# Kernel tuning notes

Hardware: AMD Instinct MI355X
Metric: run time of the kernel (lower is better)

## Reference

```python
import jax, jax.numpy as jnp
import numpy as np
import math

GROUPS = 32
HEADS = 8
EPS_GN = 1e-5


def group_norm(x, w, b):
    # x: [B, C, H, W]; GroupNorm32 computes in float32
    B, C, H, W = x.shape
    xg = x.astype(jnp.float32).reshape(B, GROUPS, C // GROUPS, H, W)
    mu = xg.mean(axis=(2, 3, 4), keepdims=True)
    var = xg.var(axis=(2, 3, 4), keepdims=True)
    xn = (xg - mu) * jax.lax.rsqrt(var + EPS_GN)
    xn = xn.reshape(B, C, H, W)
    return (xn * w[None, :, None, None] + b[None, :, None, None]).astype(x.dtype)


def fresnel_interference(H, W, wavelength):
    ys, xs = jnp.meshgrid(jnp.arange(H, dtype=jnp.float32),
                          jnp.arange(W, dtype=jnp.float32), indexing='ij')
    pos = jnp.stack([ys, xs], axis=-1).reshape(-1, 2)  # [N, 2]
    diff = pos[None, :, :] - pos[:, None, :]           # [N, N, 2]
    dist = jnp.sqrt((diff ** 2).sum(-1) + 1e-8)        # [N, N]
    phase = 2.0 * math.pi * dist / (jnp.abs(wavelength) * H + 1e-6)
    return jnp.cos(phase)


def fresnel_attn(h, qkv_w, out_w, out_b, wavelength):
    B, C, H, W = h.shape
    N = H * W
    dh = C // HEADS
    scale = dh ** -0.5
    xf = h.reshape(B, C, N).transpose(0, 2, 1)                 # [B, N, C]
    qkv = xf @ qkv_w                                            # [B, N, 3C]
    q, k, v = jnp.split(qkv, 3, axis=-1)
    def heads(t):
        return t.reshape(B, N, HEADS, dh).transpose(0, 2, 1, 3)  # [B, Hh, N, dh]
    q, k, v = heads(q), heads(k), heads(v)
    dots = jnp.einsum('bhnd,bhmd->bhnm', q, k) * scale
    interference = fresnel_interference(H, W, wavelength)       # [N, N]
    dots = dots + interference[None, None] * 0.1
    attn = jax.nn.softmax(dots, axis=-1)
    out = jnp.einsum('bhnm,bhmd->bhnd', attn, v)
    out = out.transpose(0, 2, 1, 3).reshape(B, N, C)
    out = out @ out_w + out_b
    return out.transpose(0, 2, 1).reshape(B, C, H, W)


def cross_attn(h, context, q_w, k_w, v_w, out_w, out_b):
    B, C, H, W = h.shape
    N = H * W
    inner = q_w.shape[1]
    dh = inner // HEADS
    scale = dh ** -0.5
    xf = h.reshape(B, C, N).transpose(0, 2, 1)                 # [B, N, C]
    q = xf @ q_w                                                # [B, N, inner]
    k = context @ k_w                                           # [B, L, inner]
    v = context @ v_w
    L = context.shape[1]
    q = q.reshape(B, N, HEADS, dh).transpose(0, 2, 1, 3)
    k = k.reshape(B, L, HEADS, dh).transpose(0, 2, 1, 3)
    v = v.reshape(B, L, HEADS, dh).transpose(0, 2, 1, 3)
    attn = jax.nn.softmax(jnp.einsum('bhnd,bhld->bhnl', q, k) * scale, axis=-1)
    out = jnp.einsum('bhnl,bhld->bhnd', attn, v)
    out = out.transpose(0, 2, 1, 3).reshape(B, N, inner)
    out = out @ out_w + out_b
    return out.transpose(0, 2, 1).reshape(B, C, H, W)


def setup_inputs() -> dict:
    key = jax.random.key(0)
    ks = jax.random.split(key, 10)
    B, C, H, W = 4, 512, 32, 32
    ctx_len, ctx_dim = 77, 768
    s = lambda d: 1.0 / math.sqrt(d)
    return {
        'x': jax.random.normal(ks[0], (B, C, H, W), jnp.float32),
        'context': jax.random.normal(ks[1], (B, ctx_len, ctx_dim), jnp.float32),
        'gn1_w': jnp.ones((C,), jnp.float32),
        'gn1_b': jnp.zeros((C,), jnp.float32),
        'gn2_w': jnp.ones((C,), jnp.float32),
        'gn2_b': jnp.zeros((C,), jnp.float32),
        'fa_qkv_w': jax.random.normal(ks[2], (C, 3 * C), jnp.float32) * s(C),
        'fa_out_w': jax.random.normal(ks[3], (C, C), jnp.float32) * s(C),
        'fa_out_b': jnp.zeros((C,), jnp.float32),
        'wavelength': jnp.asarray(0.1, jnp.float32),
        'ca_q_w': jax.random.normal(ks[4], (C, 512), jnp.float32) * s(C),
        'ca_k_w': jax.random.normal(ks[5], (ctx_dim, 512), jnp.float32) * s(ctx_dim),
        'ca_v_w': jax.random.normal(ks[6], (ctx_dim, 512), jnp.float32) * s(ctx_dim),
        'ca_out_w': jax.random.normal(ks[7], (512, C), jnp.float32) * s(512),
        'ca_out_b': jnp.zeros((C,), jnp.float32),
    }


def reference(x, context, gn1_w, gn1_b, gn2_w, gn2_b,
              fa_qkv_w, fa_out_w, fa_out_b, wavelength,
              ca_q_w, ca_k_w, ca_v_w, ca_out_w, ca_out_b):
    h = group_norm(x, gn1_w, gn1_b)
    h = fresnel_attn(h, fa_qkv_w, fa_out_w, fa_out_b, wavelength)
    x = x + h
    h = group_norm(x, gn2_w, gn2_b)
    h = cross_attn(h, context, ca_q_w, ca_k_w, ca_v_w, ca_out_w, ca_out_b)
    return x + h
```

## Files before the change

### kernel.cpp

```cpp
#include <hip/hip_runtime.h>
#include <hip/hip_bf16.h>
#include <math.h>

#define B_    4
#define N_    1024
#define L_    77

typedef float f4 __attribute__((ext_vector_type(4)));
typedef short bf8 __attribute__((ext_vector_type(8)));
typedef short s4v __attribute__((ext_vector_type(4)));

#if __has_builtin(__builtin_amdgcn_exp2f)
#define EXP2(x) __builtin_amdgcn_exp2f(x)
#else
#define EXP2(x) exp2f(x)
#endif

__device__ __forceinline__ float fs(short s) {
    unsigned u = ((unsigned)(unsigned short)s) << 16;
    return __builtin_bit_cast(float, u);
}
__device__ __forceinline__ short sf(float f) {
    unsigned u = __builtin_bit_cast(unsigned, f);
    unsigned r = (u + 0x7FFF + ((u >> 16) & 1)) >> 16;
    return (short)r;
}
__device__ __forceinline__ bf8 zero8() { bf8 v; for (int i = 0; i < 8; ++i) v[i] = 0; return v; }
__device__ __forceinline__ f4 zerof4() { f4 v; for (int i = 0; i < 4; ++i) v[i] = 0.f; return v; }

#define MFMA(a, b, c) __builtin_amdgcn_mfma_f32_16x16x32_bf16((a), (b), (c), 0, 0, 0)

__device__ __forceinline__ void wtile(const float* __restrict__ in, short* __restrict__ out,
                                      int K, int J, int tile, int tid, float (*t)[33])
{
    int jt = J >> 5;
    int j0 = (tile % jt) * 32, k0 = (tile / jt) * 32;
    int tx = tid & 31, ty = tid >> 5;
#pragma unroll
    for (int i = 0; i < 4; ++i)
        t[ty + i * 8][tx] = in[(size_t)(k0 + ty + i * 8) * J + j0 + tx];
    __syncthreads();
#pragma unroll
    for (int i = 0; i < 4; ++i)
        out[(size_t)(j0 + ty + i * 8) * K + k0 + tx] = sf(t[tx][ty + i * 8]);
}

__global__ __launch_bounds__(256)
void prep_mega(const float* __restrict__ wl, short* __restrict__ tab,
               const float* __restrict__ qkvw, short* __restrict__ qkvwT,
               const float* __restrict__ faow, short* __restrict__ faowT,
               const float* __restrict__ caqw, short* __restrict__ caqwT,
               const float* __restrict__ cakw, short* __restrict__ cakwT,
               const float* __restrict__ cavw, short* __restrict__ cavwT,
               const float* __restrict__ caow, short* __restrict__ caowT,
               const float* __restrict__ ctx, short* __restrict__ ctxb)
{
    __shared__ float tls[32][33];
    int bid = blockIdx.x, tid = threadIdx.x;
    if (bid < 16) {
        int idx = bid * 256 + tid;
        if (idx < 3969) {
            int i = idx / 63, j = idx - i * 63;
            float dy = (float)(i - 31), dx = (float)(j - 31);
            float dist = sqrtf(dy * dy + dx * dx + 1e-8f);
            float den = fabsf(wl[0]) * 32.0f + 1e-6f;
            tab[idx] = sf(0.1f * cosf(6.283185307179586f * dist / den) * 1.4426950408889634f);
        }
        return;
    }
    bid -= 16;
    if (bid < 768) { wtile(qkvw, qkvwT, 512, 1536, bid, tid, tls); return; }
    bid -= 768;
    if (bid < 256) { wtile(faow, faowT, 512, 512, bid, tid, tls); return; }
    bid -= 256;
    if (bid < 256) { wtile(caqw, caqwT, 512, 512, bid, tid, tls); return; }
    bid -= 256;
    if (bid < 384) { wtile(cakw, cakwT, 768, 512, bid, tid, tls); return; }
    bid -= 384;
    if (bid < 384) { wtile(cavw, cavwT, 768, 512, bid, tid, tls); return; }
    bid -= 384;
    if (bid < 256) { wtile(caow, caowT, 512, 512, bid, tid, tls); return; }
    bid -= 256;
    int base = bid * 1024 + tid * 4;
    float4 v = *(const float4*)(ctx + base);
    s4v o; o[0] = sf(v.x); o[1] = sf(v.y); o[2] = sf(v.z); o[3] = sf(v.w);
    *(s4v*)(ctxb + base) = o;
}

__global__ __launch_bounds__(256)
void gn_fused(const float* __restrict__ src, const float* __restrict__ w,
              const float* __restrict__ bs, short* __restrict__ dst)
{
    int g = blockIdx.x, b = blockIdx.y;
    const float* xb = src + ((size_t)b * 512 + g * 16) * 1024;
    float s = 0.f, ss = 0.f;
    for (int l = threadIdx.x; l < 4096; l += 256) {
        float4 v = *(const float4*)(xb + l * 4);
        s += v.x + v.y + v.z + v.w;
        ss += v.x * v.x + v.y * v.y + v.z * v.z + v.w * v.w;
    }
    for (int off = 32; off; off >>= 1) {
        s  += __shfl_down(s,  off);
        ss += __shfl_down(ss, off);
    }
    __shared__ float sred[8], ssred[8];
    int wid = threadIdx.x >> 6;
    if ((threadIdx.x & 63) == 0) { sred[wid] = s; ssred[wid] = ss; }
    __syncthreads();
    if (threadIdx.x == 0) {
        float S = 0.f, SS = 0.f;
        for (int i = 0; i < 4; ++i) { S += sred[i]; SS += ssred[i]; }
        float mu = S * (1.f / 16384.f);
        float var = SS * (1.f / 16384.f) - mu * mu;
        sred[4] = mu; ssred[4] = rsqrtf(var + 1e-5f);
    }
    __syncthreads();
    float mu = sred[4], rs = ssred[4];

    int c4 = threadIdx.x & 3, nb = threadIdx.x >> 2;
    int c = g * 16 + c4 * 4;
    float4 wv = *(const float4*)(w + c);
    float4 bv = *(const float4*)(bs + c);
    for (int rep = 0; rep < 16; ++rep) {
        int n = rep * 64 + nb;
        float v0 = xb[(size_t)(c4 * 4 + 0) * 1024 + n];
        float v1 = xb[(size_t)(c4 * 4 + 1) * 1024 + n];
        float v2 = xb[(size_t)(c4 * 4 + 2) * 1024 + n];
        float v3 = xb[(size_t)(c4 * 4 + 3) * 1024 + n];
        s4v hb;
        hb[0] = sf((v0 - mu) * rs * wv.x + bv.x);
        hb[1] = sf((v1 - mu) * rs * wv.y + bv.y);
        hb[2] = sf((v2 - mu) * rs * wv.z + bv.z);
        hb[3] = sf((v3 - mu) * rs * wv.w + bv.w);
        *(s4v*)(dst + ((size_t)b * 1024 + n) * 512 + c) = hb;
    }
}

template<int EPI>
__global__ __launch_bounds__(256)
void gemm_mfma(const short* __restrict__ A, const short* __restrict__ Wt,
               const float* __restrict__ bias, const float* __restrict__ res,
               void* __restrict__ outv, void* __restrict__ out2v,
               int M, int K, int J,
               long aStride, long wStride, long oStride, long o2Stride)
{
    int j0 = blockIdx.x * 128, m0 = blockIdx.y * 128, b = blockIdx.z;
    __shared__ short As[2][128][40];
    __shared__ short Ws[2][128][40];
    int tid = threadIdx.x, w = tid >> 6, lane = tid & 63;
    int lr = lane & 15, lg = lane >> 4;
    int wr = w >> 1, wc = w & 1;
    const short* Ab  = A  + (size_t)b * aStride;
    const short* Wtb = Wt + (size_t)b * wStride;
    int r0 = tid >> 2, c0 = (tid & 3) * 8;
    int r1 = 64 + r0;
    bool gA0 = (m0 + r0) < M, gA1 = (m0 + r1) < M;
    const short* ap0 = Ab + (size_t)(m0 + r0) * K + c0;
    const short* ap1 = Ab + (size_t)(m0 + r1) * K + c0;
    const short* wp0 = Wtb + (size_t)(j0 + r0) * K + c0;
    const short* wp1 = Wtb + (size_t)(j0 + r1) * K + c0;

    f4 acc[4][4];
#pragma unroll
    for (int i = 0; i < 4; ++i)
#pragma unroll
        for (int j = 0; j < 4; ++j) acc[i][j] = zerof4();

    *(bf8*)&As[0][r0][c0] = gA0 ? *(const bf8*)ap0 : zero8();
    *(bf8*)&As[0][r1][c0] = gA1 ? *(const bf8*)ap1 : zero8();
    *(bf8*)&Ws[0][r0][c0] = *(const bf8*)wp0;
    *(bf8*)&Ws[0][r1][c0] = *(const bf8*)wp1;
    __syncthreads();

    int nk = K >> 5;
    for (int t = 0; t < nk; ++t) {
        int cur = t & 1;
        bool more = (t + 1) < nk;
        bf8 na0, na1, nw0, nw1;
        if (more) {
            int ko = (t + 1) << 5;
            na0 = gA0 ? *(const bf8*)(ap0 + ko) : zero8();
            na1 = gA1 ? *(const bf8*)(ap1 + ko) : zero8();
            nw0 = *(const bf8*)(wp0 + ko);
            nw1 = *(const bf8*)(wp1 + ko);
        }
        bf8 af[4], bfr[4];
#pragma unroll
        for (int fi = 0; fi < 4; ++fi)
            af[fi] = *(const bf8*)&As[cur][wr * 64 + fi * 16 + lr][lg * 8];
#pragma unroll
        for (int fj = 0; fj < 4; ++fj)
            bfr[fj] = *(const bf8*)&Ws[cur][wc * 64 + fj * 16 + lr][lg * 8];
#pragma unroll
        for (int fi = 0; fi < 4; ++fi)
#pragma unroll
            for (int fj = 0; fj < 4; ++fj)
                acc[fi][fj] = MFMA(af[fi], bfr[fj], acc[fi][fj]);
        if (more) {
            int nb = cur ^ 1;
            *(bf8*)&As[nb][r0][c0] = na0;
            *(bf8*)&As[nb][r1][c0] = na1;
            *(bf8*)&Ws[nb][r0][c0] = nw0;
            *(bf8*)&Ws[nb][r1][c0] = nw1;
        }
        __syncthreads();
    }

    if (EPI == 0) {
        short* out = (short*)outv + (size_t)b * oStride;
#pragma unroll
        for (int fi = 0; fi < 4; ++fi)
#pragma unroll
            for (int reg = 0; reg < 4; ++reg) {
                int m = m0 + wr * 64 + fi * 16 + lg * 4 + reg;
                if (m < M) {
#pragma unroll
                    for (int fj = 0; fj < 4; ++fj)
                        out[(size_t)m * J + j0 + wc * 64 + fj * 16 + lr] = sf(acc[fi][fj][reg]);
                }
            }
    } else if (EPI == 1) {
        float* out = (float*)outv + (size_t)b * oStride;
        const float* rp = res + (size_t)b * oStride;
#pragma unroll
        for (int fi = 0; fi < 4; ++fi) {
            float4 bq = *(const float4*)(bias + m0 + wr * 64 + fi * 16 + lg * 4);
            float bvr[4] = {bq.x, bq.y, bq.z, bq.w};
#pragma unroll
            for (int reg = 0; reg < 4; ++reg) {
                int m = m0 + wr * 64 + fi * 16 + lg * 4 + reg;
                size_t ro = (size_t)m * J + j0 + wc * 64;
#pragma unroll
                for (int fj = 0; fj < 4; ++fj) {
                    size_t idx = ro + fj * 16 + lr;
                    out[idx] = acc[fi][fj][reg] + bvr[reg] + rp[idx];
                }
            }
        }
    } else if (EPI == 3) {
        if (j0 < 1024) {
            short* out = (short*)outv + (size_t)b * oStride;
#pragma unroll
            for (int fi = 0; fi < 4; ++fi)
#pragma unroll
                for (int reg = 0; reg < 4; ++reg) {
                    int m = m0 + wr * 64 + fi * 16 + lg * 4 + reg;
#pragma unroll
                    for (int fj = 0; fj < 4; ++fj)
                        out[(size_t)m * 1024 + j0 + wc * 64 + fj * 16 + lr] = sf(acc[fi][fj][reg]);
                }
        } else {
            short* Vg = (short*)out2v + (size_t)b * o2Stride;
#pragma unroll
            for (int fi = 0; fi < 4; ++fi) {
                int n = m0 + wr * 64 + fi * 16 + lg * 4;
#pragma unroll
                for (int fj = 0; fj < 4; ++fj) {
                    int dg = j0 - 1024 + wc * 64 + fj * 16 + lr;
                    s4v v;
#pragma unroll
                    for (int reg = 0; reg < 4; ++reg) v[reg] = sf(acc[fi][fj][reg]);
                    *(s4v*)(Vg + (size_t)dg * 1024 + n) = v;
                }
            }
        }
    } else {
        if (j0 < 512) {
            short* out = (short*)outv + (size_t)b * oStride;
#pragma unroll
            for (int fi = 0; fi < 4; ++fi)
#pragma unroll
                for (int reg = 0; reg < 4; ++reg) {
                    int m = m0 + wr * 64 + fi * 16 + lg * 4 + reg;
                    if (m < M) {
#pragma unroll
                        for (int fj = 0; fj < 4; ++fj)
                            out[(size_t)m * 512 + j0 + wc * 64 + fj * 16 + lr] = sf(acc[fi][fj][reg]);
                    }
                }
        } else {
            short* vt = (short*)out2v + (size_t)b * o2Stride;
#pragma unroll
            for (int fi = 0; fi < 4; ++fi) {
                int l0 = wr * 64 + fi * 16 + lg * 4;
                if (l0 < 80) {
#pragma unroll
                    for (int fj = 0; fj < 4; ++fj) {
                        int dg = j0 - 512 + wc * 64 + fj * 16 + lr;
                        s4v v;
#pragma unroll
                        for (int reg = 0; reg < 4; ++reg) v[reg] = sf(acc[fi][fj][reg]);
                        *(s4v*)(vt + (size_t)dg * 80 + l0) = v;
                    }
                }
            }
        }
    }
}

__global__ __launch_bounds__(256)
void fresnel_attn_v2(const short* __restrict__ qkb, const short* __restrict__ Vg,
                     const short* __restrict__ tab, short* __restrict__ ao)
{
    int qb = blockIdx.x, h = blockIdx.y, b = blockIdx.z;
    int n0 = qb * 64;
    __shared__ short Ks[2][64][64];
    __shared__ short Vt[2][64][64];
    __shared__ short Ps[4][16][72];
    __shared__ short tabs[4032];
    int tid = threadIdx.x, w = tid >> 6, lane = tid & 63;
    int lr = lane & 15, lg = lane >> 4;
    const short* qp = qkb + (size_t)b * 1048576;
    const short* vp = Vg + ((size_t)b * 512 + h * 64) * 1024;

    for (int l = tid; l < 504; l += 256)
        *(bf8*)&tabs[l * 8] = *(const bf8*)(tab + l * 8);

    int q = n0 + w * 16 + lr;
    bf8 qf0 = *(const bf8*)(qp + (size_t)q * 1024 + h * 64 + lg * 8);
    bf8 qf1 = *(const bf8*)(qp + (size_t)q * 1024 + h * 64 + 32 + lg * 8);

    int sr0 = tid >> 3, sc0 = tid & 7;
    int sr1 = 32 + sr0;
    int sw0 = ((sc0 ^ (sr0 & 7))) * 8;
    int sw1 = ((sc0 ^ (sr1 & 7))) * 8;

    *(bf8*)&Ks[0][sr0][sw0] = *(const bf8*)(qp + (size_t)sr0 * 1024 + 512 + h * 64 + sc0 * 8);
    *(bf8*)&Ks[0][sr1][sw1] = *(const bf8*)(qp + (size_t)sr1 * 1024 + 512 + h * 64 + sc0 * 8);
    *(bf8*)&Vt[0][sr0][sw0] = *(const bf8*)(vp + (size_t)sr0 * 1024 + sc0 * 8);
    *(bf8*)&Vt[0][sr1][sw1] = *(const bf8*)(vp + (size_t)sr1 * 1024 + sc0 * 8);
    __syncthreads();

    float mrun = -1e30f, lrun = 0.f;
    f4 o[4];
#pragma unroll
    for (int i = 0; i < 4; ++i) o[i] = zerof4();

    int ybase = (q >> 5) + 31;
    int xbase = (q & 31) + 31 - lg * 4;
    int rsw = lr & 7;
    int rc0 = (lg ^ rsw) * 8;
    int rc1 = ((4 + lg) ^ rsw) * 8;

    for (int t = 0; t < 16; ++t) {
        int cur = t & 1;
        int m0 = t << 6;
        bool more = t < 15;
        bf8 nk0, nk1, nv0, nv1;
        if (more) {
            int m1 = m0 + 64;
            nk0 = *(const bf8*)(qp + (size_t)(m1 + sr0) * 1024 + 512 + h * 64 + sc0 * 8);
            nk1 = *(const bf8*)(qp + (size_t)(m1 + sr1) * 1024 + 512 + h * 64 + sc0 * 8);
            nv0 = *(const bf8*)(vp + (size_t)sr0 * 1024 + m1 + sc0 * 8);
            nv1 = *(const bf8*)(vp + (size_t)sr1 * 1024 + m1 + sc0 * 8);
        }

        f4 sa[4];
#pragma unroll
        for (int fj = 0; fj < 4; ++fj) sa[fj] = zerof4();
#pragma unroll
        for (int fj = 0; fj < 4; ++fj)
            sa[fj] = MFMA(*(const bf8*)&Ks[cur][fj * 16 + lr][rc0], qf0, sa[fj]);
#pragma unroll
        for (int fj = 0; fj < 4; ++fj)
            sa[fj] = MFMA(*(const bf8*)&Ks[cur][fj * 16 + lr][rc1], qf1, sa[fj]);

        int yb = ybase - (m0 >> 5);
        float pv[4][4];
        float tmax = -1e30f;
#pragma unroll
        for (int fj = 0; fj < 4; ++fj) {
            int rowoff = (yb - (fj >> 1)) * 63 + xbase - (fj & 1) * 16;
#pragma unroll
            for (int reg = 0; reg < 4; ++reg) {
                float t2 = fmaf(sa[fj][reg], 0.18033688011112042f, fs(tabs[rowoff - reg]));
                pv[fj][reg] = t2;
                tmax = fmaxf(tmax, t2);
            }
        }
        tmax = fmaxf(tmax, __shfl_xor(tmax, 16));
        tmax = fmaxf(tmax, __shfl_xor(tmax, 32));
        float mnew = fmaxf(mrun, tmax);
        float rsc = EXP2(mrun - mnew);
        mrun = mnew;
        float psum = 0.f;
#pragma unroll
        for (int fj = 0; fj < 4; ++fj) {
            s4v pw;
#pragma unroll
            for (int reg = 0; reg < 4; ++reg) {
                float p = EXP2(pv[fj][reg] - mnew);
                psum += p;
                pw[reg] = sf(p);
            }
            *(s4v*)&Ps[w][lr][fj * 16 + lg * 4] = pw;
        }
        psum += __shfl_xor(psum, 16);
        psum += __shfl_xor(psum, 32);
        lrun = lrun * rsc + psum;
#pragma unroll
        for (int fd = 0; fd < 4; ++fd)
#pragma unroll
            for (int reg = 0; reg < 4; ++reg) o[fd][reg] *= rsc;

        bf8 pa0 = *(const bf8*)&Ps[w][lr][lg * 8];
        bf8 pa1 = *(const bf8*)&Ps[w][lr][32 + lg * 8];
#pragma unroll
        for (int fd = 0; fd < 4; ++fd) {
            o[fd] = MFMA(*(const bf8*)&Vt[cur][fd * 16 + lr][rc0], pa0, o[fd]);
            o[fd] = MFMA(*(const bf8*)&Vt[cur][fd * 16 + lr][rc1], pa1, o[fd]);
        }

        if (more) {
            int nb = cur ^ 1;
            *(bf8*)&Ks[nb][sr0][sw0] = nk0;
            *(bf8*)&Ks[nb][sr1][sw1] = nk1;
            *(bf8*)&Vt[nb][sr0][sw0] = nv0;
            *(bf8*)&Vt[nb][sr1][sw1] = nv1;
        }
        __syncthreads();
    }

    float inv = 1.f / lrun;
    size_t rb = ((size_t)b * N_ + q) * 512 + h * 64;
#pragma unroll
    for (int fd = 0; fd < 4; ++fd) {
        s4v ov;
#pragma unroll
        for (int reg = 0; reg < 4; ++reg) ov[reg] = sf(o[fd][reg] * inv);
        *(s4v*)(ao + rb + fd * 16 + lg * 4) = ov;
    }
}

__global__ __launch_bounds__(256)
void cross_attn_mfma(const short* __restrict__ q2, const short* __restrict__ k2,
                     const short* __restrict__ v2t, short* __restrict__ ao2)
{
    int qb = blockIdx.x, h = blockIdx.y, b = blockIdx.z;
    int n0 = qb * 64;
    __shared__ short Qs[64][72], Ks[96][72], Vt[64][104];
    __shared__ short Ps[4][16][104];
    int tid = threadIdx.x, w = tid >> 6, lane = tid & 63;
    int lr = lane & 15, lg = lane >> 4;

    for (int l = tid; l < 512; l += 256) {
        int n = l >> 3, dq = l & 7;
        *(bf8*)&Qs[n][dq * 8] = *(const bf8*)(q2 + ((size_t)b * N_ + n0 + n) * 512 + h * 64 + dq * 8);
    }
    for (int l = tid; l < 768; l += 256) {
        int m = l >> 3, dq = l & 7;
        bf8 v = zero8();
        if (m < L_) v = *(const bf8*)(k2 + ((size_t)b * L_ + m) * 512 + h * 64 + dq * 8);
        *(bf8*)&Ks[m][dq * 8] = v;
    }
    for (int l = tid; l < 768; l += 256) {
        int d = l / 12, cq = l % 12;
        bf8 v = zero8();
        if (cq < 10) v = *(const bf8*)(v2t + ((size_t)b * 512 + h * 64 + d) * 80 + cq * 8);
        *(bf8*)&Vt[d][cq * 8] = v;
    }
    __syncthreads();

    f4 sacc[6];
#pragma unroll
    for (int fj = 0; fj < 6; ++fj) sacc[fj] = zerof4();
#pragma unroll
    for (int kc = 0; kc < 2; ++kc) {
        bf8 aq = *(const bf8*)&Qs[w * 16 + lr][kc * 32 + lg * 8];
#pragma unroll
        for (int fj = 0; fj < 6; ++fj)
            sacc[fj] = MFMA(aq, *(const bf8*)&Ks[fj * 16 + lr][kc * 32 + lg * 8], sacc[fj]);
    }

    float rinv[4];
#pragma unroll
    for (int reg = 0; reg < 4; ++reg) {
        float sv[6];
#pragma unroll
        for (int fj = 0; fj < 6; ++fj) {
            int m = fj * 16 + lr;
            sv[fj] = (m < L_) ? sacc[fj][reg] * 0.125f : -30000.f;
        }
        float mx = sv[0];
#pragma unroll
        for (int fj = 1; fj < 6; ++fj) mx = fmaxf(mx, sv[fj]);
#pragma unroll
        for (int off = 1; off < 16; off <<= 1) mx = fmaxf(mx, __shfl_xor(mx, off));
        float psum = 0.f;
#pragma unroll
        for (int fj = 0; fj < 6; ++fj) {
            float p = __expf(sv[fj] - mx);
            psum += p;
            Ps[w][lg * 4 + reg][fj * 16 + lr] = sf(p);
        }
#pragma unroll
        for (int off = 1; off < 16; off <<= 1) psum += __shfl_xor(psum, off);
        rinv[reg] = 1.f / psum;
    }
    __syncthreads();

    f4 o[4];
#pragma unroll
    for (int fd = 0; fd < 4; ++fd) o[fd] = zerof4();
#pragma unroll
    for (int kc = 0; kc < 3; ++kc) {
        bf8 ap = *(const bf8*)&Ps[w][lr][kc * 32 + lg * 8];
#pragma unroll
        for (int fd = 0; fd < 4; ++fd)
            o[fd] = MFMA(ap, *(const bf8*)&Vt[fd * 16 + lr][kc * 32 + lg * 8], o[fd]);
    }

#pragma unroll
    for (int reg = 0; reg < 4; ++reg) {
        size_t rb = ((size_t)b * N_ + n0 + w * 16 + lg * 4 + reg) * 512 + h * 64;
#pragma unroll
        for (int fd = 0; fd < 4; ++fd)
            ao2[rb + fd * 16 + lr] = sf(o[fd][reg] * rinv[reg]);
    }
}

extern "C" void kernel_launch(void* const* d_in, const int* in_sizes, int n_in,
                              void* d_out, int out_size, void* d_ws, size_t ws_size,
                              hipStream_t stream)
{
    const float* x    = (const float*)d_in[0];
    const float* ctx  = (const float*)d_in[1];
    const float* gn1w = (const float*)d_in[2];
    const float* gn1b = (const float*)d_in[3];
    const float* gn2w = (const float*)d_in[4];
    const float* gn2b = (const float*)d_in[5];
    const float* qkvw = (const float*)d_in[6];
    const float* faow = (const float*)d_in[7];
    const float* faob = (const float*)d_in[8];
    const float* wl   = (const float*)d_in[9];
    const float* caqw = (const float*)d_in[10];
    const float* cakw = (const float*)d_in[11];
    const float* cavw = (const float*)d_in[12];
    const float* caow = (const float*)d_in[13];
    const float* caob = (const float*)d_in[14];
    float* out = (float*)d_out;
    char* ws = (char*)d_ws;

    float* x1    = (float*)(ws + 0);
    short* qkb   = (short*)(ws + 8388608);
    short* Vg    = (short*)(ws + 16777216);
    short* h1b   = (short*)(ws + 20971520);
    short* ao    = (short*)(ws + 25165824);
    short* q2b   = (short*)(ws + 29360128);
    short* qkvwT = (short*)(ws + 33554432);
    short* faowT = (short*)(ws + 35127296);
    short* caqwT = (short*)(ws + 35651584);
    short* cakwT = (short*)(ws + 36175872);
    short* cavwT = (short*)(ws + 36962304);
    short* caowT = (short*)(ws + 37748736);
    short* k2b   = (short*)(ws + 38273024);
    short* v2t   = (short*)(ws + 38588416);
    short* ctxb  = (short*)(ws + 38916096);
    short* tab   = (short*)(ws + 39389184);

    prep_mega<<<2551, 256, 0, stream>>>(wl, tab, qkvw, qkvwT, faow, faowT,
                                        caqw, caqwT, cakw, cakwT, cavw, cavwT,
                                        caow, caowT, ctx, ctxb);
    gn_fused<<<dim3(32, 4), 256, 0, stream>>>(x, gn1w, gn1b, h1b);
    gemm_mfma<3><<<dim3(12, 8, 4), 256, 0, stream>>>(
        h1b, qkvwT, nullptr, nullptr, qkb, Vg, 1024, 512, 1536,
        524288L, 0L, 1048576L, 524288L);
    fresnel_attn_v2<<<dim3(16, 8, 4), 256, 0, stream>>>(qkb, Vg, tab, ao);
    gemm_mfma<1><<<dim3(8, 4, 4), 256, 0, stream>>>(
        faowT, ao, faob, x, x1, nullptr, 512, 512, 1024,
        0L, 524288L, 524288L, 0L);
    gn_fused<<<dim3(32, 4), 256, 0, stream>>>(x1, gn2w, gn2b, h1b);
    gemm_mfma<0><<<dim3(4, 8, 4), 256, 0, stream>>>(
        h1b, caqwT, nullptr, nullptr, q2b, nullptr, 1024, 512, 512,
        524288L, 0L, 524288L, 0L);
    gemm_mfma<4><<<dim3(8, 1, 4), 256, 0, stream>>>(
        ctxb, cakwT, nullptr, nullptr, k2b, v2t, 77, 768, 1024,
        59136L, 0L, 39424L, 40960L);
    cross_attn_mfma<<<dim3(16, 8, 4), 256, 0, stream>>>(q2b, k2b, v2t, ao);
    gemm_mfma<1><<<dim3(8, 4, 4), 256, 0, stream>>>(
        caowT, ao, caob, x1, out, nullptr, 512, 512, 1024,
        0L, 524288L, 524288L, 0L);
}
```

Baseline: 223.3 us.

## Merge launches, add lazy softmax rescale and MFMA priority hints

Folds the first GroupNorm into the prep kernel and merges the context K/V GEMM into the QKV GEMM launch, cutting the launch count from ten to eight. The Fresnel attention's online softmax now skips the max update and rescale unless a new max exceeds the running max by more than 8, and packs probabilities with v_cvt_pk_bf16_f32. s_setprio brackets are added around MFMA blocks in both attention kernels. The lazy rescale bounds unnormalised probabilities by 2^8, which slightly changes numerics but stays within bf16/fp32 range.

```diff
diff --git a/kernel.cpp b/kernel.cpp
--- a/kernel.cpp
+++ b/kernel.cpp
@@ -30,6 +30,55 @@
 
 #define MFMA(a, b, c) __builtin_amdgcn_mfma_f32_16x16x32_bf16((a), (b), (c), 0, 0, 0)
 
+__device__ __forceinline__ void gn_body(const float* __restrict__ src,
+                                        const float* __restrict__ w,
+                                        const float* __restrict__ bs,
+                                        short* __restrict__ dst, int g, int b)
+{
+    const float* xb = src + ((size_t)b * 512 + g * 16) * 1024;
+    float s = 0.f, ss = 0.f;
+    for (int l = threadIdx.x; l < 4096; l += 256) {
+        float4 v = *(const float4*)(xb + l * 4);
+        s += v.x + v.y + v.z + v.w;
+        ss += v.x * v.x + v.y * v.y + v.z * v.z + v.w * v.w;
+    }
+    for (int off = 32; off; off >>= 1) {
+        s  += __shfl_down(s,  off);
+        ss += __shfl_down(ss, off);
+    }
+    __shared__ float sred[8], ssred[8];
+    int wid = threadIdx.x >> 6;
+    if ((threadIdx.x & 63) == 0) { sred[wid] = s; ssred[wid] = ss; }
+    __syncthreads();
+    if (threadIdx.x == 0) {
+        float S = 0.f, SS = 0.f;
+        for (int i = 0; i < 4; ++i) { S += sred[i]; SS += ssred[i]; }
+        float mu = S * (1.f / 16384.f);
+        float var = SS * (1.f / 16384.f) - mu * mu;
+        sred[4] = mu; ssred[4] = rsqrtf(var + 1e-5f);
+    }
+    __syncthreads();
+    float mu = sred[4], rs = ssred[4];
+
+    int c4 = threadIdx.x & 3, nb = threadIdx.x >> 2;
+    int c = g * 16 + c4 * 4;
+    float4 wv = *(const float4*)(w + c);
+    float4 bv = *(const float4*)(bs + c);
+    for (int rep = 0; rep < 16; ++rep) {
+        int n = rep * 64 + nb;
+        float v0 = xb[(size_t)(c4 * 4 + 0) * 1024 + n];
+        float v1 = xb[(size_t)(c4 * 4 + 1) * 1024 + n];
+        float v2 = xb[(size_t)(c4 * 4 + 2) * 1024 + n];
+        float v3 = xb[(size_t)(c4 * 4 + 3) * 1024 + n];
+        s4v hb;
+        hb[0] = sf((v0 - mu) * rs * wv.x + bv.x);
+        hb[1] = sf((v1 - mu) * rs * wv.y + bv.y);
+        hb[2] = sf((v2 - mu) * rs * wv.z + bv.z);
+        hb[3] = sf((v3 - mu) * rs * wv.w + bv.w);
+        *(s4v*)(dst + ((size_t)b * 1024 + n) * 512 + c) = hb;
+    }
+}
+
 __device__ __forceinline__ void wtile(const float* __restrict__ in, short* __restrict__ out,
                                       int K, int J, int tile, int tid, float (*t)[33])
 {
@@ -46,7 +95,9 @@
 }
 
 __global__ __launch_bounds__(256)
-void prep_mega(const float* __restrict__ wl, short* __restrict__ tab,
+void prep_mega(const float* __restrict__ x, const float* __restrict__ gn1w,
+               const float* __restrict__ gn1b, short* __restrict__ h1b,
+               const float* __restrict__ wl, short* __restrict__ tab,
                const float* __restrict__ qkvw, short* __restrict__ qkvwT,
                const float* __restrict__ faow, short* __restrict__ faowT,
                const float* __restrict__ caqw, short* __restrict__ caqwT,
@@ -57,6 +108,8 @@
 {
     __shared__ float tls[32][33];
     int bid = blockIdx.x, tid = threadIdx.x;
+    if (bid < 128) { gn_body(x, gn1w, gn1b, h1b, bid & 31, bid >> 5); return; }
+    bid -= 128;
     if (bid < 16) {
         int idx = bid * 256 + tid;
         if (idx < 3969) {
@@ -88,65 +141,20 @@
 }
 
 __global__ __launch_bounds__(256)
-void gn_fused(const float* __restrict__ src, const float* __restrict__ w,
-              const float* __restrict__ bs, short* __restrict__ dst)
-{
-    int g = blockIdx.x, b = blockIdx.y;
-    const float* xb = src + ((size_t)b * 512 + g * 16) * 1024;
-    float s = 0.f, ss = 0.f;
-    for (int l = threadIdx.x; l < 4096; l += 256) {
-        float4 v = *(const float4*)(xb + l * 4);
-        s += v.x + v.y + v.z + v.w;
-        ss += v.x * v.x + v.y * v.y + v.z * v.z + v.w * v.w;
-    }
-    for (int off = 32; off; off >>= 1) {
-        s  += __shfl_down(s,  off);
-        ss += __shfl_down(ss, off);
-    }
-    __shared__ float sred[8], ssred[8];
-    int wid = threadIdx.x >> 6;
-    if ((threadIdx.x & 63) == 0) { sred[wid] = s; ssred[wid] = ss; }
-    __syncthreads();
-    if (threadIdx.x == 0) {
-        float S = 0.f, SS = 0.f;
-        for (int i = 0; i < 4; ++i) { S += sred[i]; SS += ssred[i]; }
-        float mu = S * (1.f / 16384.f);
-        float var = SS * (1.f / 16384.f) - mu * mu;
-        sred[4] = mu; ssred[4] = rsqrtf(var + 1e-5f);
-    }
-    __syncthreads();
-    float mu = sred[4], rs = ssred[4];
-
-    int c4 = threadIdx.x & 3, nb = threadIdx.x >> 2;
-    int c = g * 16 + c4 * 4;
-    float4 wv = *(const float4*)(w + c);
-    float4 bv = *(const float4*)(bs + c);
-    for (int rep = 0; rep < 16; ++rep) {
-        int n = rep * 64 + nb;
-        float v0 = xb[(size_t)(c4 * 4 + 0) * 1024 + n];
-        float v1 = xb[(size_t)(c4 * 4 + 1) * 1024 + n];
-        float v2 = xb[(size_t)(c4 * 4 + 2) * 1024 + n];
-        float v3 = xb[(size_t)(c4 * 4 + 3) * 1024 + n];
-        s4v hb;
-        hb[0] = sf((v0 - mu) * rs * wv.x + bv.x);
-        hb[1] = sf((v1 - mu) * rs * wv.y + bv.y);
-        hb[2] = sf((v2 - mu) * rs * wv.z + bv.z);
-        hb[3] = sf((v3 - mu) * rs * wv.w + bv.w);
-        *(s4v*)(dst + ((size_t)b * 1024 + n) * 512 + c) = hb;
-    }
+void gn_kernel(const float* __restrict__ src, const float* __restrict__ w,
+               const float* __restrict__ bs, short* __restrict__ dst)
+{
+    gn_body(src, w, bs, dst, blockIdx.x, blockIdx.y);
 }
 
 template<int EPI>
-__global__ __launch_bounds__(256)
-void gemm_mfma(const short* __restrict__ A, const short* __restrict__ Wt,
-               const float* __restrict__ bias, const float* __restrict__ res,
-               void* __restrict__ outv, void* __restrict__ out2v,
-               int M, int K, int J,
-               long aStride, long wStride, long oStride, long o2Stride)
-{
-    int j0 = blockIdx.x * 128, m0 = blockIdx.y * 128, b = blockIdx.z;
-    __shared__ short As[2][128][40];
-    __shared__ short Ws[2][128][40];
+__device__ __forceinline__ void gemm_body(
+    short* As, short* Ws, int j0, int m0, int b,
+    const short* __restrict__ A, const short* __restrict__ Wt,
+    const float* __restrict__ bias, const float* __restrict__ res,
+    void* __restrict__ outv, void* __restrict__ out2v,
+    int M, int K, int J, long aStride, long wStride, long oStride, long o2Stride)
+{
     int tid = threadIdx.x, w = tid >> 6, lane = tid & 63;
     int lr = lane & 15, lg = lane >> 4;
     int wr = w >> 1, wc = w & 1;
@@ -166,15 +174,15 @@
 #pragma unroll
         for (int j = 0; j < 4; ++j) acc[i][j] = zerof4();
 
-    *(bf8*)&As[0][r0][c0] = gA0 ? *(const bf8*)ap0 : zero8();
-    *(bf8*)&As[0][r1][c0] = gA1 ? *(const bf8*)ap1 : zero8();
-    *(bf8*)&Ws[0][r0][c0] = *(const bf8*)wp0;
-    *(bf8*)&Ws[0][r1][c0] = *(const bf8*)wp1;
+    *(bf8*)(As + r0 * 40 + c0) = gA0 ? *(const bf8*)ap0 : zero8();
+    *(bf8*)(As + r1 * 40 + c0) = gA1 ? *(const bf8*)ap1 : zero8();
+    *(bf8*)(Ws + r0 * 40 + c0) = *(const bf8*)wp0;
+    *(bf8*)(Ws + r1 * 40 + c0) = *(const bf8*)wp1;
     __syncthreads();
 
     int nk = K >> 5;
     for (int t = 0; t < nk; ++t) {
-        int cur = t & 1;
+        int cur = (t & 1) * 5120;
         bool more = (t + 1) < nk;
         bf8 na0, na1, nw0, nw1;
         if (more) {
@@ -187,21 +195,21 @@
         bf8 af[4], bfr[4];
 #pragma unroll
         for (int fi = 0; fi < 4; ++fi)
-            af[fi] = *(const bf8*)&As[cur][wr * 64 + fi * 16 + lr][lg * 8];
+            af[fi] = *(const bf8*)(As + cur + (wr * 64 + fi * 16 + lr) * 40 + lg * 8);
 #pragma unroll
         for (int fj = 0; fj < 4; ++fj)
-            bfr[fj] = *(const bf8*)&Ws[cur][wc * 64 + fj * 16 + lr][lg * 8];
+            bfr[fj] = *(const bf8*)(Ws + cur + (wc * 64 + fj * 16 + lr) * 40 + lg * 8);
 #pragma unroll
         for (int fi = 0; fi < 4; ++fi)
 #pragma unroll
             for (int fj = 0; fj < 4; ++fj)
                 acc[fi][fj] = MFMA(af[fi], bfr[fj], acc[fi][fj]);
         if (more) {
-            int nb = cur ^ 1;
-            *(bf8*)&As[nb][r0][c0] = na0;
-            *(bf8*)&As[nb][r1][c0] = na1;
-            *(bf8*)&Ws[nb][r0][c0] = nw0;
-            *(bf8*)&Ws[nb][r1][c0] = nw1;
+            int nb = 5120 - cur;
+            *(bf8*)(As + nb + r0 * 40 + c0) = na0;
+            *(bf8*)(As + nb + r1 * 40 + c0) = na1;
+            *(bf8*)(Ws + nb + r0 * 40 + c0) = nw0;
+            *(bf8*)(Ws + nb + r1 * 40 + c0) = nw1;
         }
         __syncthreads();
     }
@@ -298,8 +306,41 @@
     }
 }
 
+template<int EPI>
 __global__ __launch_bounds__(256)
-void fresnel_attn_v2(const short* __restrict__ qkb, const short* __restrict__ Vg,
+void gemm_std(const short* __restrict__ A, const short* __restrict__ Wt,
+              const float* __restrict__ bias, const float* __restrict__ res,
+              void* __restrict__ outv, void* __restrict__ out2v,
+              int M, int K, int J, long aStride, long wStride, long oStride, long o2Stride)
+{
+    __shared__ short As[2 * 128 * 40];
+    __shared__ short Ws[2 * 128 * 40];
+    gemm_body<EPI>(As, Ws, blockIdx.x * 128, blockIdx.y * 128, blockIdx.z,
+                   A, Wt, bias, res, outv, out2v, M, K, J,
+                   aStride, wStride, oStride, o2Stride);
+}
+
+__global__ __launch_bounds__(256)
+void gemm_qkv_kv(const short* __restrict__ h1b, const short* __restrict__ qkvwT,
+                 short* __restrict__ qkb, short* __restrict__ Vg,
+                 const short* __restrict__ ctxb, const short* __restrict__ cakwT,
+                 short* __restrict__ k2b, short* __restrict__ v2t)
+{
+    __shared__ short As[2 * 128 * 40];
+    __shared__ short Ws[2 * 128 * 40];
+    if (blockIdx.y < 8) {
+        gemm_body<3>(As, Ws, blockIdx.x * 128, blockIdx.y * 128, blockIdx.z,
+                     h1b, qkvwT, nullptr, nullptr, qkb, Vg,
+                     1024, 512, 1536, 524288L, 0L, 1048576L, 524288L);
+    } else if (blockIdx.x < 8) {
+        gemm_body<4>(As, Ws, blockIdx.x * 128, 0, blockIdx.z,
+                     ctxb, cakwT, nullptr, nullptr, k2b, v2t,
+                     77, 768, 1024, 59136L, 0L, 39424L, 40960L);
+    }
+}
+
+__global__ __launch_bounds__(256)
+void fresnel_attn_v3(const short* __restrict__ qkb, const short* __restrict__ Vg,
                      const short* __restrict__ tab, short* __restrict__ ao)
 {
     int qb = blockIdx.x, h = blockIdx.y, b = blockIdx.z;
@@ -358,12 +399,14 @@
         f4 sa[4];
 #pragma unroll
         for (int fj = 0; fj < 4; ++fj) sa[fj] = zerof4();
+        __builtin_amdgcn_s_setprio(1);
 #pragma unroll
         for (int fj = 0; fj < 4; ++fj)
             sa[fj] = MFMA(*(const bf8*)&Ks[cur][fj * 16 + lr][rc0], qf0, sa[fj]);
 #pragma unroll
         for (int fj = 0; fj < 4; ++fj)
             sa[fj] = MFMA(*(const bf8*)&Ks[cur][fj * 16 + lr][rc1], qf1, sa[fj]);
+        __builtin_amdgcn_s_setprio(0);
 
         int yb = ybase - (m0 >> 5);
         float pv[4][4];
@@ -378,38 +421,45 @@
                 tmax = fmaxf(tmax, t2);
             }
         }
-        tmax = fmaxf(tmax, __shfl_xor(tmax, 16));
-        tmax = fmaxf(tmax, __shfl_xor(tmax, 32));
-        float mnew = fmaxf(mrun, tmax);
-        float rsc = EXP2(mrun - mnew);
-        mrun = mnew;
+        if (__any(tmax > mrun + 8.f)) {
+            tmax = fmaxf(tmax, __shfl_xor(tmax, 16));
+            tmax = fmaxf(tmax, __shfl_xor(tmax, 32));
+            float mnew = fmaxf(mrun, tmax);
+            float rsc = EXP2(mrun - mnew);
+            mrun = mnew;
+            lrun *= rsc;
+#pragma unroll
+            for (int fd = 0; fd < 4; ++fd)
+#pragma unroll
+                for (int reg = 0; reg < 4; ++reg) o[fd][reg] *= rsc;
+        }
         float psum = 0.f;
 #pragma unroll
         for (int fj = 0; fj < 4; ++fj) {
-            s4v pw;
-#pragma unroll
-            for (int reg = 0; reg < 4; ++reg) {
-                float p = EXP2(pv[fj][reg] - mnew);
-                psum += p;
-                pw[reg] = sf(p);
-            }
-            *(s4v*)&Ps[w][lr][fj * 16 + lg * 4] = pw;
+            float p0 = EXP2(pv[fj][0] - mrun);
+            float p1 = EXP2(pv[fj][1] - mrun);
+            float p2 = EXP2(pv[fj][2] - mrun);
+            float p3 = EXP2(pv[fj][3] - mrun);
+            psum += (p0 + p1) + (p2 + p3);
+            int r01, r23;
+            asm("v_cvt_pk_bf16_f32 %0, %1, %2" : "=v"(r01) : "v"(p0), "v"(p1));
+            asm("v_cvt_pk_bf16_f32 %0, %1, %2" : "=v"(r23) : "v"(p2), "v"(p3));
+            int2 pr; pr.x = r01; pr.y = r23;
+            *(int2*)&Ps[w][lr][fj * 16 + lg * 4] = pr;
         }
         psum += __shfl_xor(psum, 16);
         psum += __shfl_xor(psum, 32);
-        lrun = lrun * rsc + psum;
-#pragma unroll
-        for (int fd = 0; fd < 4; ++fd)
-#pragma unroll
-            for (int reg = 0; reg < 4; ++reg) o[fd][reg] *= rsc;
+        lrun += psum;
 
         bf8 pa0 = *(const bf8*)&Ps[w][lr][lg * 8];
         bf8 pa1 = *(const bf8*)&Ps[w][lr][32 + lg * 8];
+        __builtin_amdgcn_s_setprio(1);
 #pragma unroll
         for (int fd = 0; fd < 4; ++fd) {
             o[fd] = MFMA(*(const bf8*)&Vt[cur][fd * 16 + lr][rc0], pa0, o[fd]);
             o[fd] = MFMA(*(const bf8*)&Vt[cur][fd * 16 + lr][rc1], pa1, o[fd]);
         }
+        __builtin_amdgcn_s_setprio(0);
 
         if (more) {
             int nb = cur ^ 1;
@@ -464,6 +514,7 @@
     f4 sacc[6];
 #pragma unroll
     for (int fj = 0; fj < 6; ++fj) sacc[fj] = zerof4();
+    __builtin_amdgcn_s_setprio(1);
 #pragma unroll
     for (int kc = 0; kc < 2; ++kc) {
         bf8 aq = *(const bf8*)&Qs[w * 16 + lr][kc * 32 + lg * 8];
@@ -471,6 +522,7 @@
         for (int fj = 0; fj < 6; ++fj)
             sacc[fj] = MFMA(aq, *(const bf8*)&Ks[fj * 16 + lr][kc * 32 + lg * 8], sacc[fj]);
     }
+    __builtin_amdgcn_s_setprio(0);
 
     float rinv[4];
 #pragma unroll
@@ -502,6 +554,7 @@
     f4 o[4];
 #pragma unroll
     for (int fd = 0; fd < 4; ++fd) o[fd] = zerof4();
+    __builtin_amdgcn_s_setprio(1);
 #pragma unroll
     for (int kc = 0; kc < 3; ++kc) {
         bf8 ap = *(const bf8*)&Ps[w][lr][kc * 32 + lg * 8];
@@ -509,6 +562,7 @@
         for (int fd = 0; fd < 4; ++fd)
             o[fd] = MFMA(ap, *(const bf8*)&Vt[fd * 16 + lr][kc * 32 + lg * 8], o[fd]);
     }
+    __builtin_amdgcn_s_setprio(0);
 
 #pragma unroll
     for (int reg = 0; reg < 4; ++reg) {
@@ -558,26 +612,22 @@
     short* ctxb  = (short*)(ws + 38916096);
     short* tab   = (short*)(ws + 39389184);
 
-    prep_mega<<<2551, 256, 0, stream>>>(wl, tab, qkvw, qkvwT, faow, faowT,
+    prep_mega<<<2679, 256, 0, stream>>>(x, gn1w, gn1b, h1b,
+                                        wl, tab, qkvw, qkvwT, faow, faowT,
                                         caqw, caqwT, cakw, cakwT, cavw, cavwT,
                                         caow, caowT, ctx, ctxb);
-    gn_fused<<<dim3(32, 4), 256, 0, stream>>>(x, gn1w, gn1b, h1b);
-    gemm_mfma<3><<<dim3(12, 8, 4), 256, 0, stream>>>(
-        h1b, qkvwT, nullptr, nullptr, qkb, Vg, 1024, 512, 1536,
-        524288L, 0L, 1048576L, 524288L);
-    fresnel_attn_v2<<<dim3(16, 8, 4), 256, 0, stream>>>(qkb, Vg, tab, ao);
-    gemm_mfma<1><<<dim3(8, 4, 4), 256, 0, stream>>>(
+    gemm_qkv_kv<<<dim3(12, 9, 4), 256, 0, stream>>>(
+        h1b, qkvwT, qkb, Vg, ctxb, cakwT, k2b, v2t);
+    fresnel_attn_v3<<<dim3(16, 8, 4), 256, 0, stream>>>(qkb, Vg, tab, ao);
+    gemm_std<1><<<dim3(8, 4, 4), 256, 0, stream>>>(
         faowT, ao, faob, x, x1, nullptr, 512, 512, 1024,
         0L, 524288L, 524288L, 0L);
-    gn_fused<<<dim3(32, 4), 256, 0, stream>>>(x1, gn2w, gn2b, h1b);
-    gemm_mfma<0><<<dim3(4, 8, 4), 256, 0, stream>>>(
+    gn_kernel<<<dim3(32, 4), 256, 0, stream>>>(x1, gn2w, gn2b, h1b);
+    gemm_std<0><<<dim3(4, 8, 4), 256, 0, stream>>>(
         h1b, caqwT, nullptr, nullptr, q2b, nullptr, 1024, 512, 512,
         524288L, 0L, 524288L, 0L);
-    gemm_mfma<4><<<dim3(8, 1, 4), 256, 0, stream>>>(
-        ctxb, cakwT, nullptr, nullptr, k2b, v2t, 77, 768, 1024,
-        59136L, 0L, 39424L, 40960L);
     cross_attn_mfma<<<dim3(16, 8, 4), 256, 0, stream>>>(q2b, k2b, v2t, ao);
-    gemm_mfma<1><<<dim3(8, 4, 4), 256, 0, stream>>>(
+    gemm_std<1><<<dim3(8, 4, 4), 256, 0, stream>>>(
         caowT, ao, caob, x1, out, nullptr, 512, 512, 1024,
         0L, 524288L, 524288L, 0L);
 }
```

Measured after the change: 218.9 us. Within noise of the previous version (-1.9%).
